# Optimization experiments

Hardware: AMD Instinct MI355X
Metric: run time of the kernel (lower is better)

## Reference

```python
import jax, jax.numpy as jnp
import numpy as np

N, E, G, D, OUT, VOCAB = 100000, 1600000, 512, 128, 10, 500
BN_EPS = 1e-5


def _lin(h, W, b):
    return h @ W + b


def _mlp(h, W1, b1, W2, b2):
    return _lin(jax.nn.relu(_lin(h, W1, b1)), W2, b2)


def _bn(h, g, b):
    mu = jnp.mean(h, axis=0)
    var = jnp.var(h, axis=0)
    return (h - mu) * jax.lax.rsqrt(var + BN_EPS) * g + b


def setup_inputs() -> dict:
    key = jax.random.key(0)
    ks = jax.random.split(key, 32)
    s = 1.0 / np.sqrt(D)
    inp = {
        'x': jax.random.randint(ks[0], (N,), 0, VOCAB, dtype=jnp.int32),
        'edge_index': jax.random.randint(ks[1], (2, E), 0, N, dtype=jnp.int32),
        'batch': jnp.sort(jax.random.randint(ks[2], (N,), 0, G, dtype=jnp.int32)),
        'emb': jax.random.normal(ks[3], (VOCAB, D), jnp.float32),
        'iw1': jax.random.normal(ks[4], (D, D), jnp.float32) * s,
        'ib1': jnp.zeros((D,), jnp.float32),
        'iw2': jax.random.normal(ks[5], (D, D), jnp.float32) * s,
        'ib2': jnp.zeros((D,), jnp.float32),
        'f1w': jax.random.normal(ks[6], (D, D), jnp.float32) * s,
        'f1b': jnp.zeros((D,), jnp.float32),
        'f2w': jax.random.normal(ks[7], (D, OUT), jnp.float32) * s,
        'f2b': jnp.zeros((OUT,), jnp.float32),
    }
    for i, base in zip(range(3), (8, 14, 20)):
        l = i + 1
        inp[f'c{l}w1'] = jax.random.normal(ks[base], (D, D), jnp.float32) * s
        inp[f'c{l}b1'] = jnp.zeros((D,), jnp.float32)
        inp[f'c{l}w2'] = jax.random.normal(ks[base + 1], (D, D), jnp.float32) * s
        inp[f'c{l}b2'] = jnp.zeros((D,), jnp.float32)
        inp[f'g{l}'] = jnp.ones((D,), jnp.float32)
        inp[f'be{l}'] = jnp.zeros((D,), jnp.float32)
    return inp


def reference(x, edge_index, batch,
              emb, iw1, ib1, iw2, ib2,
              c1w1, c1b1, c1w2, c1b2, g1, be1,
              c2w1, c2b1, c2w2, c2b2, g2, be2,
              c3w1, c3b1, c3w2, c3b2, g3, be3,
              f1w, f1b, f2w, f2b):
    src, dst = edge_index[0], edge_index[1]

    def gin_conv(h, W1, b1, W2, b2):
        # scatter-add neighbor aggregation, eps = 0 -> (1+0)*x + sum_j x_j
        agg = jax.ops.segment_sum(h[src], dst, num_segments=N)
        return _mlp(h + agg, W1, b1, W2, b2)

    h = emb[x]                                   # [N, D] embedding lookup
    h = _mlp(h, iw1, ib1, iw2, ib2)              # initial_mlp
    h = jax.nn.relu(_bn(gin_conv(h, c1w1, c1b1, c1w2, c1b2), g1, be1))
    h = jax.nn.relu(_bn(gin_conv(h, c2w1, c2b1, c2w2, c2b2), g2, be2))
    h = jax.nn.relu(_bn(gin_conv(h, c3w1, c3b1, c3w2, c3b2), g3, be3))
    p = jax.ops.segment_sum(h, batch, num_segments=G)   # global_add_pool [G, D]
    p = jax.nn.relu(_lin(p, f1w, f1b))
    # dropout in eval mode = identity
    return _lin(p, f2w, f2b)                     # [G, OUT]
```

## Files before the change

kernel.cpp:

```cpp
#include <hip/hip_runtime.h>

typedef unsigned short u16;
typedef unsigned int u32;
typedef __bf16 bf16x8 __attribute__((ext_vector_type(8)));
typedef float f32x4 __attribute__((ext_vector_type(4)));

#define MFMA_BF16(a, b, c) __builtin_amdgcn_mfma_f32_16x16x32_bf16(a, b, c, 0, 0, 0)

#define NBUC_MAX 512
#define BCAP 4608
#define EPB 8192

__device__ __forceinline__ float bf2f(u16 h) {
  u32 u = ((u32)h) << 16;
  return __builtin_bit_cast(float, u);
}
__device__ __forceinline__ u16 f2bf(float f) {
  u32 u = __builtin_bit_cast(u32, f);
  u += 0x7fffu + ((u >> 16) & 1u);
  return (u16)(u >> 16);
}

__global__ __launch_bounds__(256) void prep_w6(const float* __restrict__ w0,
                                               const float* __restrict__ w1,
                                               const float* __restrict__ w2,
                                               const float* __restrict__ w3,
                                               const float* __restrict__ w4,
                                               const float* __restrict__ w5,
                                               u16* __restrict__ wt) {
  const int which = blockIdx.x >> 6;
  const float* w = which == 0 ? w0 : which == 1 ? w1 : which == 2 ? w2
                  : which == 3 ? w3 : which == 4 ? w4 : w5;
  int t = (blockIdx.x & 63) * 256 + threadIdx.x;
  int n = t >> 7, k = t & 127;
  wt[which * 16384 + n * 128 + k] = f2bf(w[k * 128 + n]);
}

__global__ __launch_bounds__(128) void mlp0_table(
    const float* __restrict__ emb, const float* __restrict__ w1, const float* __restrict__ b1,
    const float* __restrict__ w2, const float* __restrict__ b2, u16* __restrict__ table) {
  __shared__ float e[128];
  __shared__ float tt[128];
  int r = blockIdx.x, j = threadIdx.x;
  e[j] = emb[r * 128 + j];
  __syncthreads();
  float s = b1[j];
  for (int k = 0; k < 128; ++k) s += e[k] * w1[k * 128 + j];
  tt[j] = s > 0.f ? s : 0.f;
  __syncthreads();
  float s2 = b2[j];
  for (int k = 0; k < 128; ++k) s2 += tt[k] * w2[k * 128 + j];
  table[r * 128 + j] = f2bf(s2);
}

__global__ __launch_bounds__(256) void bucket_scatter(const int* __restrict__ src,
                                                      const int* __restrict__ dst,
                                                      u32* __restrict__ pairs,
                                                      u32* __restrict__ cursor, int E_, int nbuc) {
  __shared__ u32 sv[EPB];
  __shared__ u16 sb[EPB];
  __shared__ u32 lcnt[NBUC_MAX];
  __shared__ u32 lbase[NBUC_MAX];
  const int t = threadIdx.x;
  for (int b = t; b < NBUC_MAX; b += 256) lcnt[b] = 0;
  __syncthreads();
  const int e0 = blockIdx.x * EPB;
#pragma unroll
  for (int it = 0; it < EPB / 256; ++it) {
    int idx = it * 256 + t;
    int e = e0 + idx;
    u32 v = 0u;
    u16 b = 0xffffu;
    if (e < E_) {
      int s = src[e], d = dst[e];
      b = (u16)(d >> 8);
      v = ((u32)s << 8) | (u32)(d & 255);
      atomicAdd(&lcnt[b], 1u);
    }
    sv[idx] = v;
    sb[idx] = b;
  }
  __syncthreads();
  for (int b = t; b < nbuc; b += 256) {
    u32 c = lcnt[b];
    lbase[b] = c ? atomicAdd(&cursor[b], c) : 0u;
    lcnt[b] = 0;
  }
  __syncthreads();
#pragma unroll
  for (int it = 0; it < EPB / 256; ++it) {
    int idx = it * 256 + t;
    u16 b = sb[idx];
    if (b != 0xffffu) {
      u32 r = atomicAdd(&lcnt[b], 1u);
      u32 p = lbase[b] + r;
      if (p < BCAP) pairs[(size_t)b * BCAP + p] = sv[idx];
    }
  }
}

__global__ __launch_bounds__(256) void csr_build(const u32* __restrict__ pairs,
                                                 const u32* __restrict__ cursor,
                                                 u32* __restrict__ csr, int* __restrict__ RS,
                                                 int* __restrict__ DEG, int nrows) {
  __shared__ u32 cnt[256];
  __shared__ u32 offs[256];
  __shared__ u32 basearr[256];
  const int b = blockIdx.x, t = threadIdx.x;
  u32 count = cursor[b];
  if (count > BCAP) count = BCAP;
  cnt[t] = 0;
  __syncthreads();
  const u32* pb = pairs + (size_t)b * BCAP;
  for (u32 i = t; i < count; i += 256) atomicAdd(&cnt[pb[i] & 255u], 1u);
  __syncthreads();
  const u32 my = cnt[t];
  offs[t] = my;
  __syncthreads();
  for (int d = 1; d < 256; d <<= 1) {
    u32 v = (t >= d) ? offs[t - d] : 0u;
    __syncthreads();
    offs[t] += v;
    __syncthreads();
  }
  const u32 excl = offs[t] - my;
  const int node = (b << 8) + t;
  if (node < nrows) {
    RS[node] = b * BCAP + (int)excl;
    DEG[node] = (int)my;
  }
  basearr[t] = excl;
  cnt[t] = 0;
  __syncthreads();
  for (u32 i = t; i < count; i += 256) {
    u32 v = pb[i];
    u32 dl = v & 255u;
    u32 r = atomicAdd(&cnt[dl], 1u);
    csr[(size_t)b * BCAP + basearr[dl] + r] = v >> 8;
  }
}

template <int MODE>
__global__ __launch_bounds__(256) void agg_kernel(
    const u16* __restrict__ Hsrc, const int* __restrict__ x, const u32* __restrict__ csr,
    const int* __restrict__ RS, const int* __restrict__ DEG, const float* __restrict__ stats,
    const float* __restrict__ g, const float* __restrict__ be, float invN,
    u16* __restrict__ AGG, int nrows) {
  __shared__ float ssc[256];
  const int t = threadIdx.x;
  if (MODE == 1) {
    if (t < 128) {
      float mu = stats[t] * invN;
      float var = stats[128 + t] * invN - mu * mu;
      float rstd = rsqrtf(var + 1e-5f);
      float s = rstd * g[t];
      ssc[t] = s;
      ssc[128 + t] = be[t] - mu * s;
    }
    __syncthreads();
  }
  int node = blockIdx.x * 4 + (t >> 6);
  if (node >= nrows) return;
  const int lane = t & 63;
  const int grp = lane >> 4;
  const int fl = lane & 15;
  const int deg = DEG[node];
  const u32* cl = csr + RS[node];

  float sc[8], sh[8];
  if (MODE == 1) {
#pragma unroll
    for (int i = 0; i < 8; ++i) {
      sc[i] = ssc[fl * 8 + i];
      sh[i] = ssc[128 + fl * 8 + i];
    }
  }
  float a[8];
#pragma unroll
  for (int i = 0; i < 8; ++i) a[i] = 0.f;

#define ACCUM(vv)                                   \
  {                                                 \
    const u16* p = (const u16*)&(vv);               \
    _Pragma("unroll") for (int i = 0; i < 8; ++i) { \
      float xv = bf2f(p[i]);                        \
      if (MODE == 1) {                              \
        xv = xv * sc[i] + sh[i];                    \
        xv = xv > 0.f ? xv : 0.f;                   \
      }                                             \
      a[i] += xv;                                   \
    }                                               \
  }
#define ROWPTR(idx) (Hsrc + (size_t)(MODE == 0 ? x[idx] : (idx)) * 128 + fl * 8)

  if (grp == 0) {
    uint4 v = *(const uint4*)ROWPTR(node);
    ACCUM(v);
  }
  int j = grp;
  bool okA = j < deg, okB = j + 4 < deg;
  uint4 vA = make_uint4(0u, 0u, 0u, 0u), vB = make_uint4(0u, 0u, 0u, 0u);
  if (okA) vA = *(const uint4*)ROWPTR((int)cl[j]);
  if (okB) vB = *(const uint4*)ROWPTR((int)cl[j + 4]);
  while (okA) {
    const bool okC = j + 8 < deg, okD = j + 12 < deg;
    const int iC = okC ? (int)cl[j + 8] : 0;
    const int iD = okD ? (int)cl[j + 12] : 0;
    uint4 a0 = vA, a1 = vB;
    const bool o1 = okB;
    vA = make_uint4(0u, 0u, 0u, 0u);
    vB = make_uint4(0u, 0u, 0u, 0u);
    if (okC) vA = *(const uint4*)ROWPTR(iC);
    if (okD) vB = *(const uint4*)ROWPTR(iD);
    ACCUM(a0);
    if (o1) ACCUM(a1);
    okA = okC;
    okB = okD;
    j += 8;
  }
#undef ROWPTR
#undef ACCUM

#pragma unroll
  for (int i = 0; i < 8; ++i) {
    a[i] += __shfl_xor(a[i], 16);
    a[i] += __shfl_xor(a[i], 32);
  }
  if (grp == 0) {
    u32 o[4];
#pragma unroll
    for (int i = 0; i < 4; ++i) o[i] = (u32)f2bf(a[2 * i]) | ((u32)f2bf(a[2 * i + 1]) << 16);
    *(uint4*)(AGG + (size_t)node * 128 + fl * 8) = *(uint4*)o;
  }
}

__global__ __launch_bounds__(256) void mlp_kernel(
    const u16* __restrict__ X, const u16* __restrict__ W1t, const float* __restrict__ b1,
    const u16* __restrict__ W2t, const float* __restrict__ b2, u16* __restrict__ Y,
    float* __restrict__ stats, int nrows) {
  __shared__ u16 Xs[64 * 136];
  __shared__ u16 Ts[64 * 136];
  const int t = threadIdx.x;
  const int row0 = blockIdx.x * 64;
  {
    const int seg = t & 15;
    const int rb = t >> 4;
#pragma unroll
    for (int p = 0; p < 4; ++p) {
      const int r = rb + p * 16;
      const int gr = row0 + r;
      uint4 v = make_uint4(0u, 0u, 0u, 0u);
      if (gr < nrows) v = *(const uint4*)(X + (size_t)gr * 128 + seg * 8);
      *(uint4*)(Xs + r * 136 + seg * 8) = v;
    }
  }
  __syncthreads();
  const int lane = t & 63;
  const int wave = t >> 6;
  const int n0 = wave * 32;
  const int nl = lane & 15;
  const int quad = lane >> 4;

  bf16x8 bw[2][4];
#pragma unroll
  for (int nt = 0; nt < 2; ++nt)
#pragma unroll
    for (int kk = 0; kk < 4; ++kk)
      bw[nt][kk] = *(const bf16x8*)(W1t + (size_t)(n0 + nt * 16 + nl) * 128 + kk * 32 + quad * 8);

  f32x4 acc[4][2];
#pragma unroll
  for (int mt = 0; mt < 4; ++mt) {
    acc[mt][0] = (f32x4)0.0f;
    acc[mt][1] = (f32x4)0.0f;
  }
#pragma unroll
  for (int kk = 0; kk < 4; ++kk) {
#pragma unroll
    for (int mt = 0; mt < 4; ++mt) {
      bf16x8 a = *(const bf16x8*)(Xs + (mt * 16 + nl) * 136 + kk * 32 + quad * 8);
      acc[mt][0] = MFMA_BF16(a, bw[0][kk], acc[mt][0]);
      acc[mt][1] = MFMA_BF16(a, bw[1][kk], acc[mt][1]);
    }
  }
#pragma unroll
  for (int nt = 0; nt < 2; ++nt) {
    const int n = n0 + nt * 16 + nl;
    const float bias = b1[n];
#pragma unroll
    for (int mt = 0; mt < 4; ++mt)
#pragma unroll
      for (int r = 0; r < 4; ++r) {
        float v = acc[mt][nt][r] + bias;
        v = v > 0.f ? v : 0.f;
        Ts[(mt * 16 + quad * 4 + r) * 136 + n] = f2bf(v);
      }
  }
  __syncthreads();
#pragma unroll
  for (int nt = 0; nt < 2; ++nt)
#pragma unroll
    for (int kk = 0; kk < 4; ++kk)
      bw[nt][kk] = *(const bf16x8*)(W2t + (size_t)(n0 + nt * 16 + nl) * 128 + kk * 32 + quad * 8);
#pragma unroll
  for (int mt = 0; mt < 4; ++mt) {
    acc[mt][0] = (f32x4)0.0f;
    acc[mt][1] = (f32x4)0.0f;
  }
#pragma unroll
  for (int kk = 0; kk < 4; ++kk) {
#pragma unroll
    for (int mt = 0; mt < 4; ++mt) {
      bf16x8 a = *(const bf16x8*)(Ts + (mt * 16 + nl) * 136 + kk * 32 + quad * 8);
      acc[mt][0] = MFMA_BF16(a, bw[0][kk], acc[mt][0]);
      acc[mt][1] = MFMA_BF16(a, bw[1][kk], acc[mt][1]);
    }
  }
  float ssum[2] = {0.f, 0.f}, ssq[2] = {0.f, 0.f};
#pragma unroll
  for (int nt = 0; nt < 2; ++nt) {
    const int n = n0 + nt * 16 + nl;
    const float bias = b2[n];
#pragma unroll
    for (int mt = 0; mt < 4; ++mt)
#pragma unroll
      for (int r = 0; r < 4; ++r) {
        const int row = row0 + mt * 16 + quad * 4 + r;
        float v = acc[mt][nt][r] + bias;
        if (row < nrows) {
          Y[(size_t)row * 128 + n] = f2bf(v);
          ssum[nt] += v;
          ssq[nt] += v * v;
        }
      }
  }
#pragma unroll
  for (int nt = 0; nt < 2; ++nt) {
    float s = ssum[nt], q = ssq[nt];
    s += __shfl_xor(s, 16);
    q += __shfl_xor(q, 16);
    s += __shfl_xor(s, 32);
    q += __shfl_xor(q, 32);
    if (quad == 0) {
      const int n = n0 + nt * 16 + nl;
      atomicAdd(&stats[n], s);
      atomicAdd(&stats[128 + n], q);
    }
  }
}

__global__ __launch_bounds__(256) void pool_final(
    const u16* __restrict__ Hh, const int* __restrict__ batch, const float* __restrict__ stats,
    const float* __restrict__ g, const float* __restrict__ be, float invN,
    const float* __restrict__ f1w, const float* __restrict__ f1b, const float* __restrict__ f2w,
    const float* __restrict__ f2b, float* __restrict__ out, int nrows) {
  __shared__ float ssc[256];
  __shared__ float red[16][128];
  __shared__ float pr[128];
  __shared__ float tt[128];
  const int gid = blockIdx.x, t = threadIdx.x;
  if (t < 128) {
    float mu = stats[t] * invN;
    float var = stats[128 + t] * invN - mu * mu;
    float rstd = rsqrtf(var + 1e-5f);
    float s = rstd * g[t];
    ssc[t] = s;
    ssc[128 + t] = be[t] - mu * s;
  }
  __syncthreads();
  int l = 0, r = nrows;
  while (l < r) {
    int m = (l + r) >> 1;
    if (batch[m] < gid) l = m + 1; else r = m;
  }
  const int s0 = l;
  r = nrows;
  while (l < r) {
    int m = (l + r) >> 1;
    if (batch[m] < gid + 1) l = m + 1; else r = m;
  }
  const int s1 = l;
  const int fl = t & 15;
  const int grp = t >> 4;
  float sc[8], sh[8];
#pragma unroll
  for (int i = 0; i < 8; ++i) {
    sc[i] = ssc[fl * 8 + i];
    sh[i] = ssc[128 + fl * 8 + i];
  }
  float a[8];
#pragma unroll
  for (int i = 0; i < 8; ++i) a[i] = 0.f;
  for (int i = s0 + grp; i < s1; i += 16) {
    uint4 v = *(const uint4*)(Hh + (size_t)i * 128 + fl * 8);
    const u16* pp = (const u16*)&v;
#pragma unroll
    for (int k = 0; k < 8; ++k) {
      float xv = bf2f(pp[k]) * sc[k] + sh[k];
      a[k] += xv > 0.f ? xv : 0.f;
    }
  }
#pragma unroll
  for (int k = 0; k < 8; ++k) red[grp][fl * 8 + k] = a[k];
  __syncthreads();
  if (t < 128) {
    float s = 0.f;
#pragma unroll
    for (int gg2 = 0; gg2 < 16; ++gg2) s += red[gg2][t];
    pr[t] = s;
  }
  __syncthreads();
  if (t < 128) {
    float s = f1b[t];
    for (int k = 0; k < 128; ++k) s += pr[k] * f1w[k * 128 + t];
    tt[t] = s > 0.f ? s : 0.f;
  }
  __syncthreads();
  if (t < 10) {
    float s2 = f2b[t];
    for (int k = 0; k < 128; ++k) s2 += tt[k] * f2w[k * 10 + t];
    out[gid * 10 + t] = s2;
  }
}

extern "C" void kernel_launch(void* const* d_in, const int* in_sizes, int n_in, void* d_out,
                              int out_size, void* d_ws, size_t ws_size, hipStream_t stream) {
  const int* x = (const int*)d_in[0];
  const int* ei = (const int*)d_in[1];
  const int* batch = (const int*)d_in[2];
  const float* emb = (const float*)d_in[3];
  const float* iw1 = (const float*)d_in[4];
  const float* ib1 = (const float*)d_in[5];
  const float* iw2 = (const float*)d_in[6];
  const float* ib2 = (const float*)d_in[7];
  const float* f1w = (const float*)d_in[8];
  const float* f1b = (const float*)d_in[9];
  const float* f2w = (const float*)d_in[10];
  const float* f2b = (const float*)d_in[11];
  const float* cw1[3] = {(const float*)d_in[12], (const float*)d_in[18], (const float*)d_in[24]};
  const float* cb1[3] = {(const float*)d_in[13], (const float*)d_in[19], (const float*)d_in[25]};
  const float* cw2[3] = {(const float*)d_in[14], (const float*)d_in[20], (const float*)d_in[26]};
  const float* cb2[3] = {(const float*)d_in[15], (const float*)d_in[21], (const float*)d_in[27]};
  const float* gg[3] = {(const float*)d_in[16], (const float*)d_in[22], (const float*)d_in[28]};
  const float* bb[3] = {(const float*)d_in[17], (const float*)d_in[23], (const float*)d_in[29]};

  const int N_ = in_sizes[0];
  const int E_ = in_sizes[1] / 2;
  const int V_ = in_sizes[3] / 128;
  const int G_ = out_size / 10;
  const int NBUC = (N_ + 255) >> 8;
  const float invN = 1.0f / (float)N_;

  char* ws = (char*)d_ws;
  u16* H = (u16*)(ws + 0);
  u16* AGG = (u16*)(ws + 25600000);
  u32* PAIRS = (u32*)(ws + 51200000);
  u32* CSR = (u32*)(ws + 60637184);
  int* RS = (int*)(ws + 70074368);
  int* DEG = (int*)(ws + 70474368);
  u32* CUR = (u32*)(ws + 70874368);
  float* STATS = (float*)(ws + 70876416);
  u16* WT = (u16*)(ws + 70882560);
  u16* TBL = (u16*)(ws + 71079168);

  hipMemsetAsync(ws + 70874368, 0, 5120, stream);

  prep_w6<<<384, 256, 0, stream>>>(cw1[0], cw2[0], cw1[1], cw2[1], cw1[2], cw2[2], WT);
  mlp0_table<<<V_, 128, 0, stream>>>(emb, iw1, ib1, iw2, ib2, TBL);
  bucket_scatter<<<(E_ + EPB - 1) / EPB, 256, 0, stream>>>(ei, ei + E_, PAIRS, CUR, E_, NBUC);
  csr_build<<<NBUC, 256, 0, stream>>>(PAIRS, CUR, CSR, RS, DEG, N_);

  const int ablk = (N_ + 3) / 4;
  const int mblk = (N_ + 63) / 64;
  for (int l = 0; l < 3; ++l) {
    const u16* W1 = WT + (size_t)l * 32768;
    const u16* W2 = WT + (size_t)l * 32768 + 16384;
    if (l == 0)
      agg_kernel<0><<<ablk, 256, 0, stream>>>(TBL, x, CSR, RS, DEG, nullptr, nullptr, nullptr,
                                              invN, AGG, N_);
    else
      agg_kernel<1><<<ablk, 256, 0, stream>>>(H, nullptr, CSR, RS, DEG, STATS + (l - 1) * 256,
                                              gg[l - 1], bb[l - 1], invN, AGG, N_);
    mlp_kernel<<<mblk, 256, 0, stream>>>(AGG, W1, cb1[l], W2, cb2[l], H, STATS + l * 256, N_);
  }
  pool_final<<<G_, 256, 0, stream>>>(H, batch, STATS + 2 * 256, gg[2], bb[2], invN, f1w, f1b,
                                     f2w, f2b, (float*)d_out, N_);
}
```

Before: 555.4 us.

## Replace BN stat atomics with per-block partials and a reduce kernel; simplify gather

The MLP kernel now writes per-block partial sums and squared sums instead of issuing global float atomics into a shared stats buffer. A new single-block bn_reduce kernel folds those partials into scale/shift vectors once per layer, so the aggregation and pool kernels no longer recompute BN parameters per block or need a __syncthreads. The neighbor gather loop is also changed from a 2-deep unrolled prefetch to a 1-deep prefetch, with 32-bit byte offsets used for row addressing. This adds an extra launch per layer and reduces memory-level parallelism in the gather.

```diff
diff --git a/kernel.cpp b/kernel.cpp
--- a/kernel.cpp
+++ b/kernel.cpp
@@ -143,36 +143,24 @@
 template <int MODE>
 __global__ __launch_bounds__(256) void agg_kernel(
     const u16* __restrict__ Hsrc, const int* __restrict__ x, const u32* __restrict__ csr,
-    const int* __restrict__ RS, const int* __restrict__ DEG, const float* __restrict__ stats,
-    const float* __restrict__ g, const float* __restrict__ be, float invN,
+    const int* __restrict__ RS, const int* __restrict__ DEG, const float* __restrict__ scsh,
     u16* __restrict__ AGG, int nrows) {
-  __shared__ float ssc[256];
-  const int t = threadIdx.x;
-  if (MODE == 1) {
-    if (t < 128) {
-      float mu = stats[t] * invN;
-      float var = stats[128 + t] * invN - mu * mu;
-      float rstd = rsqrtf(var + 1e-5f);
-      float s = rstd * g[t];
-      ssc[t] = s;
-      ssc[128 + t] = be[t] - mu * s;
-    }
-    __syncthreads();
-  }
-  int node = blockIdx.x * 4 + (t >> 6);
+  int node = blockIdx.x * 4 + (threadIdx.x >> 6);
   if (node >= nrows) return;
-  const int lane = t & 63;
+  const int lane = threadIdx.x & 63;
   const int grp = lane >> 4;
   const int fl = lane & 15;
   const int deg = DEG[node];
   const u32* cl = csr + RS[node];
+  const char* Hb = (const char*)Hsrc;
+  const u32 flo = (u32)fl << 4;
 
   float sc[8], sh[8];
   if (MODE == 1) {
 #pragma unroll
     for (int i = 0; i < 8; ++i) {
-      sc[i] = ssc[fl * 8 + i];
-      sh[i] = ssc[128 + fl * 8 + i];
+      sc[i] = scsh[fl * 8 + i];
+      sh[i] = scsh[128 + fl * 8 + i];
     }
   }
   float a[8];
@@ -191,34 +179,26 @@
       a[i] += xv;                                   \
     }                                               \
   }
-#define ROWPTR(idx) (Hsrc + (size_t)(MODE == 0 ? x[idx] : (idx)) * 128 + fl * 8)
+#define ROWOFF(idx) ((((u32)(MODE == 0 ? x[(idx)] : (idx))) << 8) + flo)
 
   if (grp == 0) {
-    uint4 v = *(const uint4*)ROWPTR(node);
+    uint4 v = *(const uint4*)(Hb + ROWOFF(node));
     ACCUM(v);
   }
   int j = grp;
-  bool okA = j < deg, okB = j + 4 < deg;
-  uint4 vA = make_uint4(0u, 0u, 0u, 0u), vB = make_uint4(0u, 0u, 0u, 0u);
-  if (okA) vA = *(const uint4*)ROWPTR((int)cl[j]);
-  if (okB) vB = *(const uint4*)ROWPTR((int)cl[j + 4]);
-  while (okA) {
-    const bool okC = j + 8 < deg, okD = j + 12 < deg;
-    const int iC = okC ? (int)cl[j + 8] : 0;
-    const int iD = okD ? (int)cl[j + 12] : 0;
-    uint4 a0 = vA, a1 = vB;
-    const bool o1 = okB;
-    vA = make_uint4(0u, 0u, 0u, 0u);
-    vB = make_uint4(0u, 0u, 0u, 0u);
-    if (okC) vA = *(const uint4*)ROWPTR(iC);
-    if (okD) vB = *(const uint4*)ROWPTR(iD);
-    ACCUM(a0);
-    if (o1) ACCUM(a1);
-    okA = okC;
-    okB = okD;
-    j += 8;
-  }
-#undef ROWPTR
+  int cA = (j < deg) ? (int)cl[j] : 0;
+  int cB = (j + 4 < deg) ? (int)cl[j + 4] : 0;
+  uint4 nv = make_uint4(0u, 0u, 0u, 0u);
+  if (j < deg) nv = *(const uint4*)(Hb + ROWOFF(cA));
+  while (j < deg) {
+    uint4 cv = nv;
+    int cn = cB;
+    cB = (j + 8 < deg) ? (int)cl[j + 8] : 0;
+    if (j + 4 < deg) nv = *(const uint4*)(Hb + ROWOFF(cn));
+    ACCUM(cv);
+    j += 4;
+  }
+#undef ROWOFF
 #undef ACCUM
 
 #pragma unroll
@@ -237,7 +217,7 @@
 __global__ __launch_bounds__(256) void mlp_kernel(
     const u16* __restrict__ X, const u16* __restrict__ W1t, const float* __restrict__ b1,
     const u16* __restrict__ W2t, const float* __restrict__ b2, u16* __restrict__ Y,
-    float* __restrict__ stats, int nrows) {
+    float* __restrict__ part, int nrows) {
   __shared__ u16 Xs[64 * 136];
   __shared__ u16 Ts[64 * 136];
   const int t = threadIdx.x;
@@ -343,31 +323,44 @@
     q += __shfl_xor(q, 32);
     if (quad == 0) {
       const int n = n0 + nt * 16 + nl;
-      atomicAdd(&stats[n], s);
-      atomicAdd(&stats[128 + n], q);
-    }
+      part[(size_t)blockIdx.x * 256 + n] = s;
+      part[(size_t)blockIdx.x * 256 + 128 + n] = q;
+    }
+  }
+}
+
+__global__ __launch_bounds__(1024) void bn_reduce(const float* __restrict__ part, int nblk,
+                                                  const float* __restrict__ g,
+                                                  const float* __restrict__ be, float invN,
+                                                  float* __restrict__ scsh) {
+  __shared__ float red[4][256];
+  const int t = threadIdx.x;
+  const int col = t & 255;
+  const int rg = t >> 8;
+  float s = 0.f;
+  for (int b = rg; b < nblk; b += 4) s += part[(size_t)b * 256 + col];
+  red[rg][col] = s;
+  __syncthreads();
+  if (rg == 0) red[0][col] = red[0][col] + red[1][col] + red[2][col] + red[3][col];
+  __syncthreads();
+  if (t < 128) {
+    float mu = red[0][t] * invN;
+    float var = red[0][128 + t] * invN - mu * mu;
+    float rstd = rsqrtf(var + 1e-5f);
+    float sc = rstd * g[t];
+    scsh[t] = sc;
+    scsh[128 + t] = be[t] - mu * sc;
   }
 }
 
 __global__ __launch_bounds__(256) void pool_final(
-    const u16* __restrict__ Hh, const int* __restrict__ batch, const float* __restrict__ stats,
-    const float* __restrict__ g, const float* __restrict__ be, float invN,
+    const u16* __restrict__ Hh, const int* __restrict__ batch, const float* __restrict__ scsh,
     const float* __restrict__ f1w, const float* __restrict__ f1b, const float* __restrict__ f2w,
     const float* __restrict__ f2b, float* __restrict__ out, int nrows) {
-  __shared__ float ssc[256];
   __shared__ float red[16][128];
   __shared__ float pr[128];
   __shared__ float tt[128];
   const int gid = blockIdx.x, t = threadIdx.x;
-  if (t < 128) {
-    float mu = stats[t] * invN;
-    float var = stats[128 + t] * invN - mu * mu;
-    float rstd = rsqrtf(var + 1e-5f);
-    float s = rstd * g[t];
-    ssc[t] = s;
-    ssc[128 + t] = be[t] - mu * s;
-  }
-  __syncthreads();
   int l = 0, r = nrows;
   while (l < r) {
     int m = (l + r) >> 1;
@@ -385,8 +378,8 @@
   float sc[8], sh[8];
 #pragma unroll
   for (int i = 0; i < 8; ++i) {
-    sc[i] = ssc[fl * 8 + i];
-    sh[i] = ssc[128 + fl * 8 + i];
+    sc[i] = scsh[fl * 8 + i];
+    sh[i] = scsh[128 + fl * 8 + i];
   }
   float a[8];
 #pragma unroll
@@ -459,11 +452,12 @@
   int* RS = (int*)(ws + 70074368);
   int* DEG = (int*)(ws + 70474368);
   u32* CUR = (u32*)(ws + 70874368);
-  float* STATS = (float*)(ws + 70876416);
-  u16* WT = (u16*)(ws + 70882560);
-  u16* TBL = (u16*)(ws + 71079168);
-
-  hipMemsetAsync(ws + 70874368, 0, 5120, stream);
+  float* SCSH = (float*)(ws + 70876416);
+  u16* WT = (u16*)(ws + 70879488);
+  u16* TBL = (u16*)(ws + 71076096);
+  float* PART = (float*)(ws + 71204096);
+
+  hipMemsetAsync(ws + 70874368, 0, 2048, stream);
 
   prep_w6<<<384, 256, 0, stream>>>(cw1[0], cw2[0], cw1[1], cw2[1], cw1[2], cw2[2], WT);
   mlp0_table<<<V_, 128, 0, stream>>>(emb, iw1, ib1, iw2, ib2, TBL);
@@ -476,13 +470,13 @@
     const u16* W1 = WT + (size_t)l * 32768;
     const u16* W2 = WT + (size_t)l * 32768 + 16384;
     if (l == 0)
-      agg_kernel<0><<<ablk, 256, 0, stream>>>(TBL, x, CSR, RS, DEG, nullptr, nullptr, nullptr,
-                                              invN, AGG, N_);
+      agg_kernel<0><<<ablk, 256, 0, stream>>>(TBL, x, CSR, RS, DEG, nullptr, AGG, N_);
     else
-      agg_kernel<1><<<ablk, 256, 0, stream>>>(H, nullptr, CSR, RS, DEG, STATS + (l - 1) * 256,
-                                              gg[l - 1], bb[l - 1], invN, AGG, N_);
-    mlp_kernel<<<mblk, 256, 0, stream>>>(AGG, W1, cb1[l], W2, cb2[l], H, STATS + l * 256, N_);
-  }
-  pool_final<<<G_, 256, 0, stream>>>(H, batch, STATS + 2 * 256, gg[2], bb[2], invN, f1w, f1b,
-                                     f2w, f2b, (float*)d_out, N_);
-}
+      agg_kernel<1><<<ablk, 256, 0, stream>>>(H, nullptr, CSR, RS, DEG, SCSH + (l - 1) * 256,
+                                              AGG, N_);
+    mlp_kernel<<<mblk, 256, 0, stream>>>(AGG, W1, cb1[l], W2, cb2[l], H, PART, N_);
+    bn_reduce<<<1, 1024, 0, stream>>>(PART, mblk, gg[l], bb[l], invN, SCSH + l * 256);
+  }
+  pool_final<<<G_, 256, 0, stream>>>(H, batch, SCSH + 2 * 256, f1w, f1b, f2w, f2b,
+                                     (float*)d_out, N_);
+}
```

Result: slower. 769.2 us (+38.5%).
